# Kernel optimization log

Measured on AMD Instinct MI355X. Metric: run time of the kernel, lower is better.

Reference implementation:

```python
import jax, jax.numpy as jnp
import numpy as np

N_POINTS = 131072  # 32 clouds * 4096 points
N_SEG = 32


def setup_inputs() -> dict:
    key = jax.random.key(0)
    ks = jax.random.split(key, 8)
    x = jax.random.normal(ks[0], (N_POINTS, 256), dtype=jnp.float32)
    pos = jax.random.normal(ks[1], (N_POINTS, 3), dtype=jnp.float32)
    # sorted segment ids, every segment non-empty (equal-size clouds)
    batch = jnp.repeat(jnp.arange(N_SEG, dtype=jnp.int32), N_POINTS // N_SEG)
    def lin(k, fan_in, fan_out):
        s = 1.0 / np.sqrt(fan_in)
        return jax.random.uniform(k, (fan_in, fan_out), jnp.float32, -s, s)
    W1 = lin(ks[2], 259, 256); b1 = jnp.zeros((256,), jnp.float32)
    W2 = lin(ks[3], 256, 512); b2 = jnp.zeros((512,), jnp.float32)
    W3 = lin(ks[4], 512, 1024); b3 = jnp.zeros((1024,), jnp.float32)
    return {"x": x, "pos": pos, "batch": batch,
            "W1": W1, "b1": b1, "W2": W2, "b2": b2, "W3": W3, "b3": b3}


def reference(x, pos, batch, W1, b1, W2, b2, W3, b3):
    # concat point features with coordinates: [N, 256+3]
    h = jnp.concatenate([x, pos], axis=1)
    # shared point-wise MLP (Linear + ReLU per layer)
    h = jax.nn.relu(h @ W1 + b1)   # [N, 256]
    h = jax.nn.relu(h @ W2 + b2)   # [N, 512]
    h = jax.nn.relu(h @ W3 + b3)   # [N, 1024]
    # global_max_pool: batch-indexed segment max -> [N_SEG, 1024]
    return jax.ops.segment_max(h, batch, num_segments=N_SEG)
```

## Files before the change

### kernel.cpp

```cpp
#include <hip/hip_runtime.h>
#include <stdint.h>

typedef unsigned short ushort_t;
typedef short shortx8 __attribute__((ext_vector_type(8)));
typedef float floatx4 __attribute__((ext_vector_type(4)));
typedef unsigned short ushortx8 __attribute__((ext_vector_type(8)));

__device__ __forceinline__ unsigned short f2bf(float f) {
  union { float f; unsigned int u; } v; v.f = f;
  unsigned int u = v.u;
  return (unsigned short)((u + 0x7fffu + ((u >> 16) & 1u)) >> 16);
}

__device__ __forceinline__ void gload_lds16(const void* g, void* l) {
  __builtin_amdgcn_global_load_lds(
      (const __attribute__((address_space(1))) unsigned int*)g,
      (__attribute__((address_space(3))) unsigned int*)l, 16, 0, 0);
}


__global__ void cvt_f32_bf16_k(const float* __restrict__ in, ushort_t* __restrict__ out, int n8) {
  int i = blockIdx.x * blockDim.x + threadIdx.x;
  if (i >= n8) return;
  const float4* p = (const float4*)in;
  float4 a = p[i * 2], b = p[i * 2 + 1];
  ushortx8 v;
  v[0] = f2bf(a.x); v[1] = f2bf(a.y); v[2] = f2bf(a.z); v[3] = f2bf(a.w);
  v[4] = f2bf(b.x); v[5] = f2bf(b.y); v[6] = f2bf(b.z); v[7] = f2bf(b.w);
  ((ushortx8*)out)[i] = v;
}

template <int K, int N>
__global__ void transpose_cvt_k(const float* __restrict__ in, ushort_t* __restrict__ out) {
  int idx = blockIdx.x * blockDim.x + threadIdx.x;
  if (idx >= N * K) return;
  int n = idx / K, k = idx - n * K;
  out[idx] = f2bf(in[k * N + n]);
}

template <int K, int NOUT, int MODE>
__global__ __launch_bounds__(256, 2) void gemm_kernel(
    const ushort_t* __restrict__ A, const ushort_t* __restrict__ BT,
    const float* __restrict__ bias, ushort_t* __restrict__ C,
    const float* __restrict__ pos, const float* __restrict__ W1tail,
    float* __restrict__ pool) {
  __shared__ __align__(16) ushort_t As[128 * 64];
  __shared__ __align__(16) ushort_t Bs[128 * 64];

  const int n0 = blockIdx.x * 128;
  const int m0 = blockIdx.y * 128;
  const int tid = threadIdx.x;
  const int w = tid >> 6;
  const int l = tid & 63;
  const int wm = w >> 1, wn = w & 1;
  const int lane16 = l & 15, lq = l >> 4;

  floatx4 acc[4][4] = {};

  const int estart = w * 512 + l * 8;
  for (int k0 = 0; k0 < K; k0 += 64) {
#pragma unroll
    for (int r = 0; r < 4; ++r) {
      int e = r * 2048 + estart;
      int row = e >> 6, col = e & 63;
      gload_lds16(A + (size_t)(m0 + row) * K + k0 + col, As + r * 2048 + w * 512);
      gload_lds16(BT + (size_t)(n0 + row) * K + k0 + col, Bs + r * 2048 + w * 512);
    }
    __syncthreads();
#pragma unroll
    for (int kk = 0; kk < 2; ++kk) {
      shortx8 af[4], bfr[4];
#pragma unroll
      for (int i = 0; i < 4; ++i)
        af[i] = *(const shortx8*)(As + (wm * 64 + i * 16 + lane16) * 64 + kk * 32 + lq * 8);
#pragma unroll
      for (int j = 0; j < 4; ++j)
        bfr[j] = *(const shortx8*)(Bs + (wn * 64 + j * 16 + lane16) * 64 + kk * 32 + lq * 8);
#pragma unroll
      for (int i = 0; i < 4; ++i)
#pragma unroll
        for (int j = 0; j < 4; ++j)
          acc[i][j] = __builtin_amdgcn_mfma_f32_16x16x32_bf16(af[i], bfr[j], acc[i][j], 0, 0, 0);
    }
    __syncthreads();
  }

  float bv[4];
#pragma unroll
  for (int j = 0; j < 4; ++j) bv[j] = bias[n0 + wn * 64 + j * 16 + lane16];

  if (MODE == 2) {
    const int seg = m0 >> 12;
#pragma unroll
    for (int j = 0; j < 4; ++j) {
      float vmax = 0.0f;
#pragma unroll
      for (int i = 0; i < 4; ++i)
#pragma unroll
        for (int r = 0; r < 4; ++r) vmax = fmaxf(vmax, acc[i][j][r] + bv[j]);
      vmax = fmaxf(vmax, __shfl_xor(vmax, 16, 64));
      vmax = fmaxf(vmax, __shfl_xor(vmax, 32, 64));
      if (l < 16) {
        int n = n0 + wn * 64 + j * 16 + lane16;
        atomicMax((int*)(pool + (size_t)seg * NOUT + n), __float_as_int(vmax));
      }
    }
  } else {
#pragma unroll
    for (int i = 0; i < 4; ++i) {
#pragma unroll
      for (int r = 0; r < 4; ++r) {
        int m = m0 + wm * 64 + i * 16 + lq * 4 + r;
        float p0 = 0.f, p1 = 0.f, p2 = 0.f;
        if (MODE == 1) { p0 = pos[m * 3 + 0]; p1 = pos[m * 3 + 1]; p2 = pos[m * 3 + 2]; }
#pragma unroll
        for (int j = 0; j < 4; ++j) {
          int n = n0 + wn * 64 + j * 16 + lane16;
          float v = acc[i][j][r] + bv[j];
          if (MODE == 1) v += p0 * W1tail[n] + p1 * W1tail[256 + n] + p2 * W1tail[512 + n];
          v = fmaxf(v, 0.0f);
          C[(size_t)m * NOUT + n] = f2bf(v);
        }
      }
    }
  }
}


extern "C" void kernel_launch(void* const* d_in, const int* in_sizes, int n_in,
                              void* d_out, int out_size, void* d_ws, size_t ws_size,
                              hipStream_t stream) {
  const float* x   = (const float*)d_in[0];
  const float* pos = (const float*)d_in[1];
  const float* W1 = (const float*)d_in[3];
  const float* b1 = (const float*)d_in[4];
  const float* W2 = (const float*)d_in[5];
  const float* b2 = (const float*)d_in[6];
  const float* W3 = (const float*)d_in[7];
  const float* b3 = (const float*)d_in[8];
  float* out = (float*)d_out;

  const int M = in_sizes[0] / 256;

  char* ws = (char*)d_ws;
  ushort_t* Xb  = (ushort_t*)ws;
  ushort_t* H2  = (ushort_t*)ws;
  ushort_t* H1  = (ushort_t*)(ws + (size_t)M * 512 * 2);
  ushort_t* W1T = (ushort_t*)(ws + (size_t)M * 512 * 2 + (size_t)M * 256 * 2);
  ushort_t* W2T = W1T + 256 * 256;
  ushort_t* W3T = W2T + 512 * 256;

  hipMemsetAsync(d_out, 0, (size_t)out_size * sizeof(float), stream);

  int n8 = M * 256 / 8;
  cvt_f32_bf16_k<<<(n8 + 255) / 256, 256, 0, stream>>>(x, Xb, n8);
  transpose_cvt_k<256, 256><<<(256 * 256 + 255) / 256, 256, 0, stream>>>(W1, W1T);
  transpose_cvt_k<256, 512><<<(512 * 256 + 255) / 256, 256, 0, stream>>>(W2, W2T);
  transpose_cvt_k<512, 1024><<<(1024 * 512 + 255) / 256, 256, 0, stream>>>(W3, W3T);

  gemm_kernel<256, 256, 1><<<dim3(2, M / 128), 256, 0, stream>>>(
      Xb, W1T, b1, H1, pos, W1 + 256 * 256, nullptr);
  gemm_kernel<256, 512, 0><<<dim3(4, M / 128), 256, 0, stream>>>(
      H1, W2T, b2, H2, nullptr, nullptr, nullptr);
  gemm_kernel<512, 1024, 2><<<dim3(8, M / 128), 256, 0, stream>>>(
      H2, W3T, b3, nullptr, nullptr, nullptr, out);
}
```

Measured before the change: 493.3 us.

## XOR-swizzle LDS tiles to remove bank conflicts and reorder grid to M-major

Each 16-byte chunk in the shared-memory A/B tiles is stored at an XOR-swizzled column (chunk ^ row&7), and the fragment reads use the same swizzle. The goal is to remove LDS bank conflicts when lanes read 16 consecutive rows at the same k offset. The grid is also swapped so blockIdx.x walks M, which changes which blocks run together and how weight and activation tiles are reused in L2. The swizzle must match exactly between the global_load_lds writes and the fragment reads.

```diff
diff --git a/kernel.cpp b/kernel.cpp
--- a/kernel.cpp
+++ b/kernel.cpp
@@ -47,35 +47,42 @@
   __shared__ __align__(16) ushort_t As[128 * 64];
   __shared__ __align__(16) ushort_t Bs[128 * 64];
 
-  const int n0 = blockIdx.x * 128;
-  const int m0 = blockIdx.y * 128;
+  const int m0 = blockIdx.x * 128;
+  const int n0 = blockIdx.y * 128;
   const int tid = threadIdx.x;
   const int w = tid >> 6;
   const int l = tid & 63;
   const int wm = w >> 1, wn = w & 1;
   const int lane16 = l & 15, lq = l >> 4;
+  const int s7 = lane16 & 7;
+
+  const int srow = l >> 3;
+  const int sg = (l & 7) ^ srow;
 
   floatx4 acc[4][4] = {};
 
-  const int estart = w * 512 + l * 8;
   for (int k0 = 0; k0 < K; k0 += 64) {
 #pragma unroll
     for (int r = 0; r < 4; ++r) {
-      int e = r * 2048 + estart;
-      int row = e >> 6, col = e & 63;
-      gload_lds16(A + (size_t)(m0 + row) * K + k0 + col, As + r * 2048 + w * 512);
-      gload_lds16(BT + (size_t)(n0 + row) * K + k0 + col, Bs + r * 2048 + w * 512);
+      const int c = r * 4 + w;
+      const int row = c * 8 + srow;
+      gload_lds16(A + (size_t)(m0 + row) * K + k0 + sg * 8, As + c * 512);
+      gload_lds16(BT + (size_t)(n0 + row) * K + k0 + sg * 8, Bs + c * 512);
     }
     __syncthreads();
 #pragma unroll
     for (int kk = 0; kk < 2; ++kk) {
       shortx8 af[4], bfr[4];
 #pragma unroll
-      for (int i = 0; i < 4; ++i)
-        af[i] = *(const shortx8*)(As + (wm * 64 + i * 16 + lane16) * 64 + kk * 32 + lq * 8);
+      for (int i = 0; i < 4; ++i) {
+        const int row = wm * 64 + i * 16 + lane16;
+        af[i] = *(const shortx8*)(As + row * 64 + ((kk * 4 + lq) ^ s7) * 8);
+      }
 #pragma unroll
-      for (int j = 0; j < 4; ++j)
-        bfr[j] = *(const shortx8*)(Bs + (wn * 64 + j * 16 + lane16) * 64 + kk * 32 + lq * 8);
+      for (int j = 0; j < 4; ++j) {
+        const int row = wn * 64 + j * 16 + lane16;
+        bfr[j] = *(const shortx8*)(Bs + row * 64 + ((kk * 4 + lq) ^ s7) * 8);
+      }
 #pragma unroll
       for (int i = 0; i < 4; ++i)
 #pragma unroll
@@ -158,10 +165,10 @@
   transpose_cvt_k<256, 512><<<(512 * 256 + 255) / 256, 256, 0, stream>>>(W2, W2T);
   transpose_cvt_k<512, 1024><<<(1024 * 512 + 255) / 256, 256, 0, stream>>>(W3, W3T);
 
-  gemm_kernel<256, 256, 1><<<dim3(2, M / 128), 256, 0, stream>>>(
+  gemm_kernel<256, 256, 1><<<dim3(M / 128, 2), 256, 0, stream>>>(
       Xb, W1T, b1, H1, pos, W1 + 256 * 256, nullptr);
-  gemm_kernel<256, 512, 0><<<dim3(4, M / 128), 256, 0, stream>>>(
+  gemm_kernel<256, 512, 0><<<dim3(M / 128, 4), 256, 0, stream>>>(
       H1, W2T, b2, H2, nullptr, nullptr, nullptr);
-  gemm_kernel<512, 1024, 2><<<dim3(8, M / 128), 256, 0, stream>>>(
+  gemm_kernel<512, 1024, 2><<<dim3(M / 128, 8), 256, 0, stream>>>(
       H2, W3T, b3, nullptr, nullptr, nullptr, out);
 }
```

Result: faster. 470.8 us (-4.6%).
